# Kernel optimization log

Hardware: AMD Instinct MI355X
Metric: run time of the kernel (lower is better)

Reference implementation:

```python
import jax, jax.numpy as jnp
import numpy as np

HIDDEN = 1024
NUM_HEADS = 16
HEAD_DIM = 64
B, S = 2, 2048


def setup_inputs() -> dict:
    key = jax.random.key(0)
    k1, k2, k3 = jax.random.split(key, 3)
    x = jax.random.normal(k1, (B, S, HIDDEN), dtype=jnp.float32)
    # xavier-uniform style scaling for the projection weights
    lim_qkv = (6.0 / (HIDDEN + 3 * NUM_HEADS * HEAD_DIM)) ** 0.5
    lim_o = (6.0 / (NUM_HEADS * HEAD_DIM + HIDDEN)) ** 0.5
    w_qkv = jax.random.uniform(k2, (HIDDEN, 3 * NUM_HEADS * HEAD_DIM), jnp.float32, -lim_qkv, lim_qkv)
    w_o = jax.random.uniform(k3, (NUM_HEADS * HEAD_DIM, HIDDEN), jnp.float32, -lim_o, lim_o)
    return {"x": x, "w_qkv": w_qkv, "w_o": w_o}


def reference(x, w_qkv, w_o):
    b, s, _ = x.shape
    qkv = jnp.einsum('bsh,hf->bsf', x, w_qkv)               # [b, s, 3*H*D]
    qkv = qkv.reshape(b, s, 3, NUM_HEADS, HEAD_DIM)
    q = jnp.transpose(qkv[:, :, 0], (0, 2, 1, 3))           # [b, h, s, d]
    k = jnp.transpose(qkv[:, :, 1], (0, 2, 3, 1))           # [b, h, d, s]
    v = jnp.transpose(qkv[:, :, 2], (0, 2, 1, 3))           # [b, h, s, d]
    scores = jnp.einsum('bhqd,bhdk->bhqk', q, k) / jnp.sqrt(jnp.float32(HEAD_DIM))
    scores = jax.nn.softmax(scores, axis=-1)                # [b, h, q, k]
    # NOTE: faithful to source bug: sums over q, output indexed by k
    values = jnp.einsum('bhqk,bhkd->bhkd', scores, v)       # [b, h, s, d]
    values = jnp.transpose(values, (0, 2, 1, 3)).reshape(b, s, NUM_HEADS * HEAD_DIM)
    return jnp.einsum('bsf,fh->bsh', values, w_o)
```

## Files before the change

### kernel.cpp

```cpp
#include <hip/hip_runtime.h>
#include <stdint.h>


#define DEV static __device__ __forceinline__

typedef unsigned short u16;
typedef __attribute__((ext_vector_type(4))) float f32x4;
typedef __attribute__((ext_vector_type(16))) float f32x16;
typedef __bf16 bf16x8 __attribute__((ext_vector_type(8)));
typedef __attribute__((ext_vector_type(8))) unsigned short u16x8;
typedef __attribute__((ext_vector_type(4))) unsigned short u16x4;

#define QSCALE 0.18033688011112042f

DEV u16 f2bf(float f) {
    unsigned u = __builtin_bit_cast(unsigned, f);
    u += 0x7fffu + ((u >> 16) & 1u);
    return (u16)(u >> 16);
}
DEV float bf2f(u16 h) {
    unsigned u = ((unsigned)h) << 16;
    return __builtin_bit_cast(float, u);
}

DEV void async_copy16(const void* g, void* l) {
    __builtin_amdgcn_global_load_lds(
        (__attribute__((address_space(1))) void*)(g),
        (__attribute__((address_space(3))) void*)(l), 16, 0, 0);
}


__global__ __launch_bounds__(256) void cast_f32_bf16(
    const float* __restrict__ src, u16* __restrict__ dst, int n4) {
    int i = blockIdx.x * 256 + threadIdx.x;
    if (i >= n4) return;
    f32x4 v = *(const f32x4*)(src + (size_t)i * 4);
    u16x4 o;
#pragma unroll
    for (int j = 0; j < 4; j++) o[j] = f2bf(v[j]);
    *(u16x4*)(dst + (size_t)i * 4) = o;
}

__global__ __launch_bounds__(256) void transpose_cast(
    const float* __restrict__ src, u16* __restrict__ dst, int rows, int cols) {
    __shared__ float tile[32][33];
    int c0 = blockIdx.x * 32, r0 = blockIdx.y * 32;
    int tx = threadIdx.x, ty = threadIdx.y;
#pragma unroll
    for (int i = 0; i < 4; i++)
        tile[ty + i * 8][tx] = src[(size_t)(r0 + ty + i * 8) * cols + c0 + tx];
    __syncthreads();
#pragma unroll
    for (int i = 0; i < 4; i++)
        dst[(size_t)(c0 + ty + i * 8) * rows + r0 + tx] = f2bf(tile[tx][ty + i * 8]);
}

__global__ __launch_bounds__(256) void gemm_qkv(
    const u16* __restrict__ A, const u16* __restrict__ Bt,
    u16* __restrict__ qb, u16* __restrict__ kb, u16* __restrict__ vb) {
    __shared__ __align__(16) u16 smem[128 * 136];
    u16* As = smem;
    u16* Bs = smem + 4096;
    const int t = threadIdx.x;
    const int wave = t >> 6;
    const int lane = t & 63;
    const int quad = lane >> 4;
    const int l16 = lane & 15;
    const int wr = wave >> 1;
    const int wc = wave & 1;
    const int m0 = blockIdx.y * 128;
    const int n0 = blockIdx.x * 128;

    f32x4 acc[4][4];
#pragma unroll
    for (int i = 0; i < 4; i++)
#pragma unroll
        for (int j = 0; j < 4; j++) acc[i][j] = {0.f, 0.f, 0.f, 0.f};

    for (int kt = 0; kt < 1024; kt += 32) {
#pragma unroll
        for (int i = 0; i < 2; i++) {
            int idx = i * 256 + t;
            int row = idx >> 2, kc = idx & 3;
            async_copy16(A + (size_t)(m0 + row) * 1024 + kt + kc * 8, &As[idx * 8]);
            async_copy16(Bt + (size_t)(n0 + row) * 1024 + kt + kc * 8, &Bs[idx * 8]);
        }
        __syncthreads();
        bf16x8 af[4], bfr[4];
#pragma unroll
        for (int mt = 0; mt < 4; mt++)
            af[mt] = *(const bf16x8*)&As[(wr * 64 + mt * 16 + l16) * 32 + quad * 8];
#pragma unroll
        for (int nt = 0; nt < 4; nt++)
            bfr[nt] = *(const bf16x8*)&Bs[(wc * 64 + nt * 16 + l16) * 32 + quad * 8];
#pragma unroll
        for (int mt = 0; mt < 4; mt++)
#pragma unroll
            for (int nt = 0; nt < 4; nt++)
                acc[mt][nt] = __builtin_amdgcn_mfma_f32_16x16x32_bf16(
                    af[mt], bfr[nt], acc[mt][nt], 0, 0, 0);
        __syncthreads();
    }

    const int tsel = n0 >> 10;
    u16* dst = tsel == 0 ? qb : (tsel == 1 ? kb : vb);
    const float scl = tsel == 0 ? QSCALE : 1.0f;
#pragma unroll
    for (int mt = 0; mt < 4; mt++)
#pragma unroll
        for (int nt = 0; nt < 4; nt++) {
            int nn = wc * 64 + nt * 16 + l16;
#pragma unroll
            for (int r = 0; r < 4; r++) {
                int mm = wr * 64 + mt * 16 + quad * 4 + r;
                smem[mm * 136 + nn] = f2bf(acc[mt][nt][r] * scl);
            }
        }
    __syncthreads();
    const int col0 = (l16) * 8;
    const int rowb = (t >> 4);
    const int h0 = (n0 & 1023) >> 6;
#pragma unroll
    for (int i = 0; i < 8; i++) {
        int row = i * 16 + rowb;
        u16x8 v = *(const u16x8*)&smem[row * 136 + col0];
        int h = h0 + (col0 >> 6), d = col0 & 63;
        int mm = m0 + row;
        int b = mm >> 11, s = mm & 2047;
        *(u16x8*)&dst[((size_t)((b * 16 + h) * 2048 + s)) * 64 + d] = v;
    }
}

__global__ __launch_bounds__(256) void gemm_out(
    const u16* __restrict__ A, const u16* __restrict__ Bt,
    float* __restrict__ out) {
    __shared__ __align__(16) u16 As[64 * 32];
    __shared__ __align__(16) u16 Bs[128 * 32];
    const int m0 = blockIdx.y * 64;
    const int n0 = blockIdx.x * 128;
    const int t = threadIdx.x;
    const int wave = t >> 6, lane = t & 63;
    const int quad = lane >> 4, l16 = lane & 15;
    const int wr = wave >> 1, wc = wave & 1;

    f32x4 acc[2][4];
#pragma unroll
    for (int i = 0; i < 2; i++)
#pragma unroll
        for (int j = 0; j < 4; j++) acc[i][j] = {0.f, 0.f, 0.f, 0.f};

    for (int kt = 0; kt < 1024; kt += 32) {
        async_copy16(A + (size_t)(m0 + (t >> 2)) * 1024 + kt + (t & 3) * 8, &As[t * 8]);
#pragma unroll
        for (int i = 0; i < 2; i++) {
            int idx = i * 256 + t;
            int row = idx >> 2, kc = idx & 3;
            async_copy16(Bt + (size_t)(n0 + row) * 1024 + kt + kc * 8, &Bs[idx * 8]);
        }
        __syncthreads();
        bf16x8 af[2], bfr[4];
#pragma unroll
        for (int mt = 0; mt < 2; mt++)
            af[mt] = *(const bf16x8*)&As[(wr * 32 + mt * 16 + l16) * 32 + quad * 8];
#pragma unroll
        for (int nt = 0; nt < 4; nt++)
            bfr[nt] = *(const bf16x8*)&Bs[(wc * 64 + nt * 16 + l16) * 32 + quad * 8];
#pragma unroll
        for (int mt = 0; mt < 2; mt++)
#pragma unroll
            for (int nt = 0; nt < 4; nt++)
                acc[mt][nt] = __builtin_amdgcn_mfma_f32_16x16x32_bf16(
                    af[mt], bfr[nt], acc[mt][nt], 0, 0, 0);
        __syncthreads();
    }
#pragma unroll
    for (int nt = 0; nt < 4; nt++) {
        int nn = n0 + wc * 64 + nt * 16 + l16;
#pragma unroll
        for (int mt = 0; mt < 2; mt++) {
#pragma unroll
            for (int r = 0; r < 4; r++) {
                int mm = m0 + wr * 32 + mt * 16 + quad * 4 + r;
                out[(size_t)mm * 1024 + nn] = acc[mt][nt][r];
            }
        }
    }
}


__global__ __launch_bounds__(256) void attn_pass1(
    const u16* __restrict__ qb, const u16* __restrict__ kb,
    float* __restrict__ lp) {
    __shared__ __align__(16) u16 Ks[2][64 * 64];
    const int t = threadIdx.x;
    const int wave = t >> 6;
    const int lane = t & 63;
    const int l32 = lane & 31, half = lane >> 5;
    const int kchunk = blockIdx.x & 3;
    const int qblk = (blockIdx.x >> 2) & 15;
    const int bh = blockIdx.x >> 6;
    const int q0 = qblk * 128 + wave * 32;

    const u16* Qr = qb + (size_t)(bh * 2048 + q0 + l32) * 64 + half * 8;
    bf16x8 a[4];
#pragma unroll
    for (int f = 0; f < 4; f++) a[f] = *(const bf16x8*)&Qr[f * 16];

    const u16* Kbase = kb + (size_t)(bh * 2048 + kchunk * 512) * 64;
    const int srow = t >> 3, sblk0 = t & 7;

    float lsum[16];
#pragma unroll
    for (int r = 0; r < 16; r++) lsum[r] = 0.f;

#define STAGE_K(buf, kt)                                                        \
    {                                                                           \
        _Pragma("unroll") for (int rr = 0; rr < 2; rr++) {                      \
            int row = rr * 32 + srow;                                           \
            int sblk = sblk0 ^ (row & 7);                                       \
            async_copy16(Kbase + (size_t)((kt) * 64 + row) * 64 + sblk * 8,     \
                         &Ks[buf][(rr * 256 + t) * 8]);                         \
        }                                                                       \
    }

    STAGE_K(0, 0);
    __syncthreads();

    for (int kt = 0; kt < 8; kt++) {
        const int cur = kt & 1;
        if (kt < 7) STAGE_K(cur ^ 1, kt + 1);
#pragma unroll
        for (int sub = 0; sub < 2; sub++) {
            const int row = sub * 32 + l32;
            const int r7 = row & 7;
            bf16x8 bfr[4];
#pragma unroll
            for (int f = 0; f < 4; f++)
                bfr[f] = *(const bf16x8*)&Ks[cur][row * 64 + ((f * 2 + half) ^ r7) * 8];
            f32x16 acc;
#pragma unroll
            for (int r = 0; r < 16; r++) acc[r] = 0.f;
            __builtin_amdgcn_s_setprio(1);
#pragma unroll
            for (int f = 0; f < 4; f++)
                acc = __builtin_amdgcn_mfma_f32_32x32x16_bf16(a[f], bfr[f], acc, 0, 0, 0);
            __builtin_amdgcn_s_setprio(0);
#pragma unroll
            for (int r = 0; r < 16; r++)
                lsum[r] += __builtin_amdgcn_exp2f(acc[r]);
        }
        __syncthreads();
    }
#pragma unroll
    for (int r = 0; r < 16; r++) {
        float v = lsum[r];
        v += __shfl_xor(v, 1);
        v += __shfl_xor(v, 2);
        v += __shfl_xor(v, 4);
        v += __shfl_xor(v, 8);
        v += __shfl_xor(v, 16);
        lsum[r] = v;
    }
    if (l32 == 0) {
        float* dst = lp + kchunk * 65536 + bh * 2048 + q0 + half * 4;
#pragma unroll
        for (int r = 0; r < 16; r++)
            dst[(r & 3) + 8 * (r >> 2)] = lsum[r];
    }
}

__global__ __launch_bounds__(256) void attn_pass2(
    const u16* __restrict__ qb, const u16* __restrict__ kb,
    const float* __restrict__ lp, float* __restrict__ cp) {
    __shared__ __align__(16) u16 Qs[2][64 * 64];
    __shared__ __align__(16) float li_lds[512];
    const int t = threadIdx.x;
    const int wave = t >> 6;
    const int lane = t & 63;
    const int l32 = lane & 31, half = lane >> 5;
    const int qchunk = blockIdx.x & 3;
    const int kblk = (blockIdx.x >> 2) & 15;
    const int bh = blockIdx.x >> 6;
    const int k0 = kblk * 128 + wave * 32;

    {
        const int base = bh * 2048 + qchunk * 512;
#pragma unroll
        for (int i = 0; i < 2; i++) {
            int q = i * 256 + t;
            float s = lp[base + q] + lp[65536 + base + q] + lp[131072 + base + q] +
                      lp[196608 + base + q];
            li_lds[q] = 1.0f / s;
        }
    }

    const u16* Kr = kb + (size_t)(bh * 2048 + k0 + l32) * 64 + half * 8;
    bf16x8 b[4];
#pragma unroll
    for (int f = 0; f < 4; f++) b[f] = *(const bf16x8*)&Kr[f * 16];

    const u16* Qbase = qb + (size_t)(bh * 2048 + qchunk * 512) * 64;
    const int srow = t >> 3, sblk0 = t & 7;

#define STAGE_Q(buf, qt)                                                        \
    {                                                                           \
        _Pragma("unroll") for (int rr = 0; rr < 2; rr++) {                      \
            int row = rr * 32 + srow;                                           \
            int sblk = sblk0 ^ (row & 7);                                       \
            async_copy16(Qbase + (size_t)((qt) * 64 + row) * 64 + sblk * 8,     \
                         &Qs[buf][(rr * 256 + t) * 8]);                         \
        }                                                                       \
    }

    float cs = 0.f;
    STAGE_Q(0, 0);
    __syncthreads();

    for (int qt = 0; qt < 8; qt++) {
        const int cur = qt & 1;
        if (qt < 7) STAGE_Q(cur ^ 1, qt + 1);
#pragma unroll
        for (int sub = 0; sub < 2; sub++) {
            const int row = sub * 32 + l32;
            const int r7 = row & 7;
            bf16x8 af[4];
#pragma unroll
            for (int f = 0; f < 4; f++)
                af[f] = *(const bf16x8*)&Qs[cur][row * 64 + ((f * 2 + half) ^ r7) * 8];
            f32x16 acc;
#pragma unroll
            for (int r = 0; r < 16; r++) acc[r] = 0.f;
            __builtin_amdgcn_s_setprio(1);
#pragma unroll
            for (int f = 0; f < 4; f++)
                acc = __builtin_amdgcn_mfma_f32_32x32x16_bf16(af[f], b[f], acc, 0, 0, 0);
            __builtin_amdgcn_s_setprio(0);
            const float* lr = &li_lds[qt * 64 + sub * 32 + half * 4];
            f32x4 li0 = *(const f32x4*)&lr[0];
            f32x4 li1 = *(const f32x4*)&lr[8];
            f32x4 li2 = *(const f32x4*)&lr[16];
            f32x4 li3 = *(const f32x4*)&lr[24];
#pragma unroll
            for (int r = 0; r < 4; r++) cs += __builtin_amdgcn_exp2f(acc[r]) * li0[r];
#pragma unroll
            for (int r = 0; r < 4; r++) cs += __builtin_amdgcn_exp2f(acc[4 + r]) * li1[r];
#pragma unroll
            for (int r = 0; r < 4; r++) cs += __builtin_amdgcn_exp2f(acc[8 + r]) * li2[r];
#pragma unroll
            for (int r = 0; r < 4; r++) cs += __builtin_amdgcn_exp2f(acc[12 + r]) * li3[r];
        }
        __syncthreads();
    }
    cs += __shfl_xor(cs, 32);
    if (lane < 32)
        cp[qchunk * 65536 + bh * 2048 + k0 + lane] = cs;
}

__global__ __launch_bounds__(256) void scale_v(
    const u16* __restrict__ vb, const float* __restrict__ cp,
    u16* __restrict__ valsb) {
    int tid = blockIdx.x * 256 + threadIdx.x;
    int base = tid << 3;
    int bh = base >> 17;
    int rem = base & 131071;
    int s = rem >> 6;
    int d0 = rem & 63;
    int ci = bh * 2048 + s;
    float cs = cp[ci] + cp[65536 + ci] + cp[131072 + ci] + cp[196608 + ci];
    u16x8 v = *(const u16x8*)(vb + (size_t)base);
    u16x8 o;
#pragma unroll
    for (int i = 0; i < 8; i++) o[i] = f2bf(bf2f(v[i]) * cs);
    int b = bh >> 4, h = bh & 15;
    *(u16x8*)&valsb[(size_t)((b * 2048 + s) * 1024) + h * 64 + d0] = o;
}


extern "C" void kernel_launch(void* const* d_in, const int* in_sizes, int n_in,
                              void* d_out, int out_size, void* d_ws, size_t ws_size,
                              hipStream_t stream) {
    const float* x    = (const float*)d_in[0];
    const float* wqkv = (const float*)d_in[1];
    const float* wo   = (const float*)d_in[2];
    float* out = (float*)d_out;
    char* ws = (char*)d_ws;

    u16* xb      = (u16*)(ws);
    u16* wqkvT   = (u16*)(ws + 8388608);
    u16* woT     = (u16*)(ws + 14680064);
    u16* qb      = (u16*)(ws + 16777216);
    u16* kb      = (u16*)(ws + 25165824);
    u16* vb      = (u16*)(ws + 33554432);
    u16* valsb   = (u16*)(ws + 42467328);
    float* lp    = (float*)(ws);
    float* cp    = (float*)(ws + 1048576);

    cast_f32_bf16<<<4096, 256, 0, stream>>>(x, xb, 1048576);
    transpose_cast<<<dim3(96, 32), dim3(32, 8), 0, stream>>>(wqkv, wqkvT, 1024, 3072);
    transpose_cast<<<dim3(32, 32), dim3(32, 8), 0, stream>>>(wo, woT, 1024, 1024);
    gemm_qkv<<<dim3(24, 32), 256, 0, stream>>>(xb, wqkvT, qb, kb, vb);
    attn_pass1<<<2048, 256, 0, stream>>>(qb, kb, lp);
    attn_pass2<<<2048, 256, 0, stream>>>(qb, kb, lp, cp);
    scale_v<<<2048, 256, 0, stream>>>(vb, cp, valsb);
    gemm_out<<<dim3(8, 64), 256, 0, stream>>>(valsb, woT, out);
}
```

Measured before the change: 202.7 us.

## Double per-wave tile in attention passes to reuse staged K/Q tiles

Each wave in both attention passes now handles two 32-row register tiles (64 rows) instead of one, and each LDS stage loads 128 rows instead of 64. Every B fragment read from LDS therefore feeds two MFMA chains, and the grid is halved to 1024 blocks. The aim is to cut LDS reads, global staging traffic and barrier count per unit of work. In exchange it uses more registers and twice the LDS per block, which may lower occupancy, and fewer blocks may leave the GPU less evenly loaded.

```diff
diff --git a/kernel.cpp b/kernel.cpp
--- a/kernel.cpp
+++ b/kernel.cpp
@@ -191,97 +191,117 @@
 __global__ __launch_bounds__(256) void attn_pass1(
     const u16* __restrict__ qb, const u16* __restrict__ kb,
     float* __restrict__ lp) {
-    __shared__ __align__(16) u16 Ks[2][64 * 64];
+    __shared__ __align__(16) u16 Ks[2][128 * 64];
     const int t = threadIdx.x;
     const int wave = t >> 6;
     const int lane = t & 63;
     const int l32 = lane & 31, half = lane >> 5;
     const int kchunk = blockIdx.x & 3;
-    const int qblk = (blockIdx.x >> 2) & 15;
-    const int bh = blockIdx.x >> 6;
-    const int q0 = qblk * 128 + wave * 32;
-
-    const u16* Qr = qb + (size_t)(bh * 2048 + q0 + l32) * 64 + half * 8;
-    bf16x8 a[4];
-#pragma unroll
-    for (int f = 0; f < 4; f++) a[f] = *(const bf16x8*)&Qr[f * 16];
+    const int qblk = (blockIdx.x >> 2) & 7;
+    const int bh = blockIdx.x >> 5;
+    const int q0 = qblk * 256 + wave * 64;
+
+    bf16x8 a[2][4];
+#pragma unroll
+    for (int qs = 0; qs < 2; qs++) {
+        const u16* Qr = qb + (size_t)(bh * 2048 + q0 + qs * 32 + l32) * 64 + half * 8;
+#pragma unroll
+        for (int f = 0; f < 4; f++) a[qs][f] = *(const bf16x8*)&Qr[f * 16];
+    }
 
     const u16* Kbase = kb + (size_t)(bh * 2048 + kchunk * 512) * 64;
-    const int srow = t >> 3, sblk0 = t & 7;
-
-    float lsum[16];
-#pragma unroll
-    for (int r = 0; r < 16; r++) lsum[r] = 0.f;
+
+    float lsum[2][16];
+#pragma unroll
+    for (int qs = 0; qs < 2; qs++)
+#pragma unroll
+        for (int r = 0; r < 16; r++) lsum[qs][r] = 0.f;
+
+    f32x16 ZZ;
+#pragma unroll
+    for (int r = 0; r < 16; r++) ZZ[r] = 0.f;
 
 #define STAGE_K(buf, kt)                                                        \
     {                                                                           \
-        _Pragma("unroll") for (int rr = 0; rr < 2; rr++) {                      \
-            int row = rr * 32 + srow;                                           \
-            int sblk = sblk0 ^ (row & 7);                                       \
-            async_copy16(Kbase + (size_t)((kt) * 64 + row) * 64 + sblk * 8,     \
-                         &Ks[buf][(rr * 256 + t) * 8]);                         \
+        _Pragma("unroll") for (int i = 0; i < 4; i++) {                         \
+            int idx = i * 256 + t;                                              \
+            int row = idx >> 3;                                                 \
+            int blk = (idx & 7) ^ (row & 7);                                    \
+            async_copy16(Kbase + (size_t)((kt) * 128 + row) * 64 + blk * 8,     \
+                         &Ks[buf][idx * 8]);                                    \
         }                                                                       \
     }
 
     STAGE_K(0, 0);
     __syncthreads();
 
-    for (int kt = 0; kt < 8; kt++) {
+    for (int kt = 0; kt < 4; kt++) {
         const int cur = kt & 1;
-        if (kt < 7) STAGE_K(cur ^ 1, kt + 1);
-#pragma unroll
-        for (int sub = 0; sub < 2; sub++) {
+        if (kt < 3) STAGE_K(cur ^ 1, kt + 1);
+#pragma unroll
+        for (int sub = 0; sub < 4; sub++) {
             const int row = sub * 32 + l32;
             const int r7 = row & 7;
             bf16x8 bfr[4];
 #pragma unroll
             for (int f = 0; f < 4; f++)
                 bfr[f] = *(const bf16x8*)&Ks[cur][row * 64 + ((f * 2 + half) ^ r7) * 8];
-            f32x16 acc;
-#pragma unroll
-            for (int r = 0; r < 16; r++) acc[r] = 0.f;
             __builtin_amdgcn_s_setprio(1);
 #pragma unroll
-            for (int f = 0; f < 4; f++)
-                acc = __builtin_amdgcn_mfma_f32_32x32x16_bf16(a[f], bfr[f], acc, 0, 0, 0);
+            for (int qs = 0; qs < 2; qs++) {
+                f32x16 acc = __builtin_amdgcn_mfma_f32_32x32x16_bf16(
+                    a[qs][0], bfr[0], ZZ, 0, 0, 0);
+#pragma unroll
+                for (int f = 1; f < 4; f++)
+                    acc = __builtin_amdgcn_mfma_f32_32x32x16_bf16(
+                        a[qs][f], bfr[f], acc, 0, 0, 0);
+                __builtin_amdgcn_s_setprio(0);
+#pragma unroll
+                for (int r = 0; r < 16; r++)
+                    lsum[qs][r] += __builtin_amdgcn_exp2f(acc[r]);
+                __builtin_amdgcn_s_setprio(1);
+            }
             __builtin_amdgcn_s_setprio(0);
+        }
+        __syncthreads();
+    }
+#pragma unroll
+    for (int qs = 0; qs < 2; qs++) {
+#pragma unroll
+        for (int r = 0; r < 16; r++) {
+            float v = lsum[qs][r];
+            v += __shfl_xor(v, 1);
+            v += __shfl_xor(v, 2);
+            v += __shfl_xor(v, 4);
+            v += __shfl_xor(v, 8);
+            v += __shfl_xor(v, 16);
+            lsum[qs][r] = v;
+        }
+    }
+    if (l32 == 0) {
+#pragma unroll
+        for (int qs = 0; qs < 2; qs++) {
+            float* dst = lp + kchunk * 65536 + bh * 2048 + q0 + qs * 32 + half * 4;
 #pragma unroll
             for (int r = 0; r < 16; r++)
-                lsum[r] += __builtin_amdgcn_exp2f(acc[r]);
-        }
-        __syncthreads();
-    }
-#pragma unroll
-    for (int r = 0; r < 16; r++) {
-        float v = lsum[r];
-        v += __shfl_xor(v, 1);
-        v += __shfl_xor(v, 2);
-        v += __shfl_xor(v, 4);
-        v += __shfl_xor(v, 8);
-        v += __shfl_xor(v, 16);
-        lsum[r] = v;
-    }
-    if (l32 == 0) {
-        float* dst = lp + kchunk * 65536 + bh * 2048 + q0 + half * 4;
-#pragma unroll
-        for (int r = 0; r < 16; r++)
-            dst[(r & 3) + 8 * (r >> 2)] = lsum[r];
+                dst[(r & 3) + 8 * (r >> 2)] = lsum[qs][r];
+        }
     }
 }
 
 __global__ __launch_bounds__(256) void attn_pass2(
     const u16* __restrict__ qb, const u16* __restrict__ kb,
     const float* __restrict__ lp, float* __restrict__ cp) {
-    __shared__ __align__(16) u16 Qs[2][64 * 64];
+    __shared__ __align__(16) u16 Qs[2][128 * 64];
     __shared__ __align__(16) float li_lds[512];
     const int t = threadIdx.x;
     const int wave = t >> 6;
     const int lane = t & 63;
     const int l32 = lane & 31, half = lane >> 5;
     const int qchunk = blockIdx.x & 3;
-    const int kblk = (blockIdx.x >> 2) & 15;
-    const int bh = blockIdx.x >> 6;
-    const int k0 = kblk * 128 + wave * 32;
+    const int kblk = (blockIdx.x >> 2) & 7;
+    const int bh = blockIdx.x >> 5;
+    const int k0 = kblk * 256 + wave * 64;
 
     {
         const int base = bh * 2048 + qchunk * 512;
@@ -294,66 +314,83 @@
         }
     }
 
-    const u16* Kr = kb + (size_t)(bh * 2048 + k0 + l32) * 64 + half * 8;
-    bf16x8 b[4];
-#pragma unroll
-    for (int f = 0; f < 4; f++) b[f] = *(const bf16x8*)&Kr[f * 16];
+    bf16x8 b[2][4];
+#pragma unroll
+    for (int ks = 0; ks < 2; ks++) {
+        const u16* Kr = kb + (size_t)(bh * 2048 + k0 + ks * 32 + l32) * 64 + half * 8;
+#pragma unroll
+        for (int f = 0; f < 4; f++) b[ks][f] = *(const bf16x8*)&Kr[f * 16];
+    }
 
     const u16* Qbase = qb + (size_t)(bh * 2048 + qchunk * 512) * 64;
-    const int srow = t >> 3, sblk0 = t & 7;
+
+    f32x16 ZZ;
+#pragma unroll
+    for (int r = 0; r < 16; r++) ZZ[r] = 0.f;
 
 #define STAGE_Q(buf, qt)                                                        \
     {                                                                           \
-        _Pragma("unroll") for (int rr = 0; rr < 2; rr++) {                      \
-            int row = rr * 32 + srow;                                           \
-            int sblk = sblk0 ^ (row & 7);                                       \
-            async_copy16(Qbase + (size_t)((qt) * 64 + row) * 64 + sblk * 8,     \
-                         &Qs[buf][(rr * 256 + t) * 8]);                         \
+        _Pragma("unroll") for (int i = 0; i < 4; i++) {                         \
+            int idx = i * 256 + t;                                              \
+            int row = idx >> 3;                                                 \
+            int blk = (idx & 7) ^ (row & 7);                                    \
+            async_copy16(Qbase + (size_t)((qt) * 128 + row) * 64 + blk * 8,     \
+                         &Qs[buf][idx * 8]);                                    \
         }                                                                       \
     }
 
-    float cs = 0.f;
+    float cs[2] = {0.f, 0.f};
     STAGE_Q(0, 0);
     __syncthreads();
 
-    for (int qt = 0; qt < 8; qt++) {
+    for (int qt = 0; qt < 4; qt++) {
         const int cur = qt & 1;
-        if (qt < 7) STAGE_Q(cur ^ 1, qt + 1);
-#pragma unroll
-        for (int sub = 0; sub < 2; sub++) {
+        if (qt < 3) STAGE_Q(cur ^ 1, qt + 1);
+#pragma unroll
+        for (int sub = 0; sub < 4; sub++) {
             const int row = sub * 32 + l32;
             const int r7 = row & 7;
             bf16x8 af[4];
 #pragma unroll
             for (int f = 0; f < 4; f++)
                 af[f] = *(const bf16x8*)&Qs[cur][row * 64 + ((f * 2 + half) ^ r7) * 8];
-            f32x16 acc;
-#pragma unroll
-            for (int r = 0; r < 16; r++) acc[r] = 0.f;
-            __builtin_amdgcn_s_setprio(1);
-#pragma unroll
-            for (int f = 0; f < 4; f++)
-                acc = __builtin_amdgcn_mfma_f32_32x32x16_bf16(af[f], b[f], acc, 0, 0, 0);
-            __builtin_amdgcn_s_setprio(0);
-            const float* lr = &li_lds[qt * 64 + sub * 32 + half * 4];
+            const float* lr = &li_lds[qt * 128 + sub * 32 + half * 4];
             f32x4 li0 = *(const f32x4*)&lr[0];
             f32x4 li1 = *(const f32x4*)&lr[8];
             f32x4 li2 = *(const f32x4*)&lr[16];
             f32x4 li3 = *(const f32x4*)&lr[24];
-#pragma unroll
-            for (int r = 0; r < 4; r++) cs += __builtin_amdgcn_exp2f(acc[r]) * li0[r];
-#pragma unroll
-            for (int r = 0; r < 4; r++) cs += __builtin_amdgcn_exp2f(acc[4 + r]) * li1[r];
-#pragma unroll
-            for (int r = 0; r < 4; r++) cs += __builtin_amdgcn_exp2f(acc[8 + r]) * li2[r];
-#pragma unroll
-            for (int r = 0; r < 4; r++) cs += __builtin_amdgcn_exp2f(acc[12 + r]) * li3[r];
-        }
-        __syncthreads();
-    }
-    cs += __shfl_xor(cs, 32);
-    if (lane < 32)
-        cp[qchunk * 65536 + bh * 2048 + k0 + lane] = cs;
+            __builtin_amdgcn_s_setprio(1);
+#pragma unroll
+            for (int ks = 0; ks < 2; ks++) {
+                f32x16 acc = __builtin_amdgcn_mfma_f32_32x32x16_bf16(
+                    af[0], b[ks][0], ZZ, 0, 0, 0);
+#pragma unroll
+                for (int f = 1; f < 4; f++)
+                    acc = __builtin_amdgcn_mfma_f32_32x32x16_bf16(
+                        af[f], b[ks][f], acc, 0, 0, 0);
+                __builtin_amdgcn_s_setprio(0);
+                float c = cs[ks];
+#pragma unroll
+                for (int r = 0; r < 4; r++) c += __builtin_amdgcn_exp2f(acc[r]) * li0[r];
+#pragma unroll
+                for (int r = 0; r < 4; r++) c += __builtin_amdgcn_exp2f(acc[4 + r]) * li1[r];
+#pragma unroll
+                for (int r = 0; r < 4; r++) c += __builtin_amdgcn_exp2f(acc[8 + r]) * li2[r];
+#pragma unroll
+                for (int r = 0; r < 4; r++) c += __builtin_amdgcn_exp2f(acc[12 + r]) * li3[r];
+                cs[ks] = c;
+                __builtin_amdgcn_s_setprio(1);
+            }
+            __builtin_amdgcn_s_setprio(0);
+        }
+        __syncthreads();
+    }
+#pragma unroll
+    for (int ks = 0; ks < 2; ks++) {
+        float v = cs[ks] + __shfl_xor(cs[ks], 32);
+        if (lane < 32)
+            cp[qchunk * 65536 + bh * 2048 + k0 + ks * 32 + lane] = v;
+    }
 }
 
 __global__ __launch_bounds__(256) void scale_v(
@@ -399,8 +436,8 @@
     transpose_cast<<<dim3(96, 32), dim3(32, 8), 0, stream>>>(wqkv, wqkvT, 1024, 3072);
     transpose_cast<<<dim3(32, 32), dim3(32, 8), 0, stream>>>(wo, woT, 1024, 1024);
     gemm_qkv<<<dim3(24, 32), 256, 0, stream>>>(xb, wqkvT, qb, kb, vb);
-    attn_pass1<<<2048, 256, 0, stream>>>(qb, kb, lp);
-    attn_pass2<<<2048, 256, 0, stream>>>(qb, kb, lp, cp);
+    attn_pass1<<<1024, 256, 0, stream>>>(qb, kb, lp);
+    attn_pass2<<<1024, 256, 0, stream>>>(qb, kb, lp, cp);
     scale_v<<<2048, 256, 0, stream>>>(vb, cp, valsb);
     gemm_out<<<dim3(8, 64), 256, 0, stream>>>(valsb, woT, out);
 }
```

After: 202.2 us. About the same (-0.3%).
